# Kernel tuning notes

Hardware: AMD Instinct MI355X
Metric: run time of the kernel (lower is better)

Reference implementation:

```python
import jax, jax.numpy as jnp
import numpy as np

B, S, D = 1, 2048, 2048
H, KV, HD = 32, 8, 64          # heads, kv heads, head_dim
WINDOW = 1024                  # sliding window (left), causal
ROPE_THETA = 10000.0


def setup_inputs() -> dict:
    key = jax.random.key(0)
    ks = jax.random.split(key, 5)
    scale = 1.0 / np.sqrt(D)
    x = jax.random.normal(ks[0], (B, S, D), dtype=jnp.float32)
    wq = jax.random.normal(ks[1], (D, H * HD), dtype=jnp.float32) * scale
    wk = jax.random.normal(ks[2], (D, KV * HD), dtype=jnp.float32) * scale
    wv = jax.random.normal(ks[3], (D, KV * HD), dtype=jnp.float32) * scale
    wo = jax.random.normal(ks[4], (H * HD, D), dtype=jnp.float32) * scale
    # RoPE frequencies: freqs_cis = exp(i * t * theta^{-2j/hd}), stored as cos/sin
    inv_freq = 1.0 / (ROPE_THETA ** (np.arange(0, HD, 2, dtype=np.float32) / HD))  # [HD/2]
    t = np.arange(S, dtype=np.float32)
    ang = np.outer(t, inv_freq)  # [S, HD/2]
    freqs_cos = jnp.asarray(np.cos(ang), dtype=jnp.float32)
    freqs_sin = jnp.asarray(np.sin(ang), dtype=jnp.float32)
    return {"x": x, "wq": wq, "wk": wk, "wv": wv, "wo": wo,
            "freqs_cos": freqs_cos, "freqs_sin": freqs_sin}


def _apply_rope(t, cos, sin):
    # t: [B,S,h,HD]; pairs (t[...,2i], t[...,2i+1]) form complex numbers
    tr = t.reshape(*t.shape[:-1], HD // 2, 2)
    a, b = tr[..., 0], tr[..., 1]
    c = cos[None, :, None, :]  # [1,S,1,HD/2]
    s = sin[None, :, None, :]
    ra = a * c - b * s
    rb = a * s + b * c
    return jnp.stack([ra, rb], axis=-1).reshape(t.shape)


def reference(x, wq, wk, wv, wo, freqs_cos, freqs_sin):
    q = (x @ wq).reshape(B, S, H, HD)
    k = (x @ wk).reshape(B, S, KV, HD)
    v = (x @ wv).reshape(B, S, KV, HD)
    q = _apply_rope(q, freqs_cos, freqs_sin)
    k = _apply_rope(k, freqs_cos, freqs_sin)
    # GQA: repeat kv heads to match query heads
    k = jnp.repeat(k, H // KV, axis=2)  # [B,S,H,HD]
    v = jnp.repeat(v, H // KV, axis=2)
    scale = jnp.asarray(1.0 / np.sqrt(HD), dtype=x.dtype)
    scores = jnp.einsum('bqhd,bkhd->bhqk', q, k) * scale  # [B,H,S,S]
    i = jnp.arange(S)[:, None]
    j = jnp.arange(S)[None, :]
    allowed = (j <= i) & (j >= i - WINDOW)  # causal + sliding window
    scores = jnp.where(allowed[None, None], scores, jnp.asarray(-1e30, dtype=scores.dtype))
    attn = jax.nn.softmax(scores, axis=-1)
    out = jnp.einsum('bhqk,bkhd->bqhd', attn, v).reshape(B, S, H * HD)
    return out @ wo
```

## Files before the change

### kernel.cpp

```cpp
#include <hip/hip_runtime.h>
#include <stdint.h>

typedef __bf16 bf16_t;
typedef __bf16 bf16x8 __attribute__((ext_vector_type(8)));
typedef __bf16 bf16x4 __attribute__((ext_vector_type(4)));
typedef float floatx4 __attribute__((ext_vector_type(4)));

#define AS3(p) ((__attribute__((address_space(3))) void*)(p))
#define AS1(p) ((__attribute__((address_space(1))) void*)(void*)(p))

__global__ __launch_bounds__(256) void cvt_k(const float* __restrict__ src,
                                             bf16_t* __restrict__ dst, int n) {
  const int i = (blockIdx.x * 256 + threadIdx.x) * 8;
  if (i + 8 <= n) {
    floatx4 a = *(const floatx4*)&src[i];
    floatx4 b = *(const floatx4*)&src[i + 4];
    bf16x8 o;
#pragma unroll
    for (int j = 0; j < 4; ++j) { o[j] = (bf16_t)a[j]; o[4 + j] = (bf16_t)b[j]; }
    *(bf16x8*)&dst[i] = o;
  }
}

__global__ __launch_bounds__(256) void tr_k(const float* __restrict__ src, int ncols,
                                            bf16_t* __restrict__ dst) {
  __shared__ __align__(16) bf16_t T[64][68];
  const int t = threadIdx.x;
  const int nt = blockIdx.x * 64, kt = blockIdx.y * 64;
  const int r0 = t >> 4;
  const int c0 = (t & 15) << 2;
#pragma unroll
  for (int p = 0; p < 4; ++p) {
    const int row = p * 16 + r0;
    floatx4 v = *(const floatx4*)&src[(size_t)(kt + row) * ncols + nt + c0];
    bf16x4 b;
#pragma unroll
    for (int i = 0; i < 4; ++i) b[i] = (bf16_t)v[i];
    *(bf16x4*)&T[row][c0] = b;
  }
  __syncthreads();
#pragma unroll
  for (int p = 0; p < 4; ++p) {
    const int n = p * 16 + r0;
    bf16x4 tmp;
#pragma unroll
    for (int i = 0; i < 4; ++i) tmp[i] = T[c0 + i][n];
    *(bf16x4*)&dst[(size_t)(nt + n) * 2048 + kt + c0] = tmp;
  }
}

template <int EPI>
__global__ __launch_bounds__(256) void gemm_k(const bf16_t* __restrict__ A,
                                              const bf16_t* __restrict__ Bt,
                                              bf16_t* __restrict__ o0,
                                              bf16_t* __restrict__ o1,
                                              bf16_t* __restrict__ o2,
                                              float* __restrict__ fo,
                                              const float* __restrict__ fcos,
                                              const float* __restrict__ fsin) {
  constexpr int K = 2048;
  __shared__ __align__(16) bf16_t As[64 * 64];
  __shared__ __align__(16) bf16_t Bs[128 * 64];
  const int tid = threadIdx.x;
  const int lane = tid & 63;
  const int w = tid >> 6;
  const int quad = lane >> 4;
  const int l15 = lane & 15;
  const int m0 = blockIdx.y * 64;
  const int n0 = blockIdx.x * 128;
  const int sr = lane >> 3;
  const int sc = ((lane & 7) ^ (sr & 7)) << 3;
  const bf16_t* gA = A + (size_t)(m0 + w * 16 + sr) * K + sc;
  const bf16_t* gB = Bt + (size_t)(n0 + w * 32 + sr) * K + sc;
  bf16_t* lA = &As[w * 1024];
  bf16_t* lB = &Bs[w * 2048];
  floatx4 acc[4][2] = {};

  for (int k0 = 0; k0 < K; k0 += 64) {
    __builtin_amdgcn_global_load_lds(AS1(gA + k0), AS3(lA), 16, 0, 0);
    __builtin_amdgcn_global_load_lds(AS1(gA + 8 * K + k0), AS3(lA + 512), 16, 0, 0);
#pragma unroll
    for (int qq = 0; qq < 4; ++qq)
      __builtin_amdgcn_global_load_lds(AS1(gB + (size_t)qq * 8 * K + k0),
                                       AS3(lB + qq * 512), 16, 0, 0);
    __syncthreads();
#pragma unroll
    for (int kk = 0; kk < 2; ++kk) {
      const int co = ((kk * 4 + quad) ^ (l15 & 7)) << 3;
      bf16x8 af[4], bfr[2];
#pragma unroll
      for (int i = 0; i < 4; ++i) af[i] = *(const bf16x8*)&As[(i * 16 + l15) * 64 + co];
#pragma unroll
      for (int i = 0; i < 2; ++i)
        bfr[i] = *(const bf16x8*)&Bs[(w * 32 + i * 16 + l15) * 64 + co];
#pragma unroll
      for (int mi = 0; mi < 4; ++mi)
#pragma unroll
        for (int ni = 0; ni < 2; ++ni)
          acc[mi][ni] =
              __builtin_amdgcn_mfma_f32_16x16x32_bf16(af[mi], bfr[ni], acc[mi][ni], 0, 0, 0);
    }
    __syncthreads();
  }

  if constexpr (EPI == 0) {
#pragma unroll
    for (int ni = 0; ni < 2; ++ni) {
      const int col = n0 + w * 32 + ni * 16 + l15;
#pragma unroll
      for (int mi = 0; mi < 4; ++mi) {
        const int sb = m0 + mi * 16 + quad * 4;
        if (col < 2560) {
          const int fi = (col & 63) >> 1;
#pragma unroll
          for (int r = 0; r < 4; ++r) {
            const float v = acc[mi][ni][r];
            const float prt = __shfl_xor(v, 1);
            const int s = sb + r;
            const float c = fcos[s * 32 + fi];
            const float sn = fsin[s * 32 + fi];
            const float ov = (col & 1) ? (prt * sn + v * c) : (v * c - prt * sn);
            if (col < 2048)
              o0[(size_t)s * 2048 + col] = (bf16_t)ov;
            else
              o1[(size_t)s * 512 + (col - 2048)] = (bf16_t)ov;
          }
        } else {
          const int sp = (sb & ~31) | (quad * 8 + (mi & 1) * 4);
          bf16x4 pv;
#pragma unroll
          for (int r = 0; r < 4; ++r) pv[r] = (bf16_t)acc[mi][ni][r];
          *(bf16x4*)&o2[(size_t)(col - 2560) * 2048 + sp] = pv;
        }
      }
    }
  } else {
#pragma unroll
    for (int ni = 0; ni < 2; ++ni) {
      const int col = n0 + w * 32 + ni * 16 + l15;
#pragma unroll
      for (int mi = 0; mi < 4; ++mi) {
        const int sb = m0 + mi * 16 + quad * 4;
#pragma unroll
        for (int r = 0; r < 4; ++r) fo[(size_t)(sb + r) * 2048 + col] = acc[mi][ni][r];
      }
    }
  }
}

__global__ __launch_bounds__(256) void attn_k(const bf16_t* __restrict__ qb_,
                                              const bf16_t* __restrict__ kb_,
                                              const bf16_t* __restrict__ vt_,
                                              bf16_t* __restrict__ ob_) {
  __shared__ __align__(16) bf16_t sm[2][8 * 512];
  const int lane = threadIdx.x & 63, w = threadIdx.x >> 6;
  const int quad = lane >> 4, l15 = lane & 15;
  const int h = blockIdx.y, g = h >> 2;
  const int qb = (gridDim.x - 1 - blockIdx.x) * 64;
  const int qw = qb + w * 16;
  const int q = qw + l15;
  const bf16_t* qrow = qb_ + (size_t)q * 2048 + h * 64;
  const bf16x8 qf0 = *(const bf16x8*)(qrow + quad * 8);
  const bf16x8 qf1 = *(const bf16x8*)(qrow + 32 + quad * 8);
  floatx4 acc0 = {}, acc1 = {}, acc2 = {}, acc3 = {}, accl = {};
  const float SC = 0.125f * 1.44269504088896340736f;
  bf16x8 ones;
#pragma unroll
  for (int i = 0; i < 8; ++i) ones[i] = (bf16_t)1.0f;

  int kbB = qb - 1024;
  if (kbB < 0) kbB = 0;
  kbB &= ~31;
  const int nT = (qb + 64 - kbB) >> 5;
  int myS = qw - 1024;
  if (myS < 0) myS = 0;
  myS &= ~31;
  const int myE = qw + 16;

  const int lr = lane & 15, lc = lane >> 4;
  const bf16_t* gk = kb_ + (size_t)(kbB + (w >> 1) * 16 + lr) * 512 + g * 64 +
                     ((w & 1) * 4 + lc) * 8;
  const bf16_t* gv = vt_ + (size_t)(g * 64 + w * 16 + lr) * 2048 + kbB + lc * 8;

#define STAGE(bi, ti)                                                              \
  do {                                                                             \
    __builtin_amdgcn_global_load_lds(AS1(gk + (size_t)(ti) * (32 * 512)),          \
                                     AS3(&sm[bi][w * 512]), 16, 0, 0);             \
    __builtin_amdgcn_global_load_lds(AS1(gv + (size_t)(ti) * 32),                  \
                                     AS3(&sm[bi][(4 + w) * 512]), 16, 0, 0);       \
  } while (0)

#define MSK(pv, key)                                        \
  do {                                                      \
    if ((key) > q || (key) + 1024 < q) pv = -1.0e30f;       \
  } while (0)

  int kb = kbB;
  STAGE(0, 0);
  __syncthreads();
  for (int i = 0; i < nT; ++i, kb += 32) {
    if (i + 1 < nT) STAGE((i + 1) & 1, i + 1);
    if (kb >= myS && kb < myE) {
      const bf16_t* base = &sm[i & 1][(size_t)lane * 8];
      const bf16x8 k0 = *(const bf16x8*)(base);
      const bf16x8 k1 = *(const bf16x8*)(base + 512);
      const bf16x8 k2 = *(const bf16x8*)(base + 1024);
      const bf16x8 k3 = *(const bf16x8*)(base + 1536);
      const bf16x8 v0 = *(const bf16x8*)(base + 2048);
      const bf16x8 v1 = *(const bf16x8*)(base + 2560);
      const bf16x8 v2 = *(const bf16x8*)(base + 3072);
      const bf16x8 v3 = *(const bf16x8*)(base + 3584);
      floatx4 z0 = {}, z1 = {};
      z0 = __builtin_amdgcn_mfma_f32_16x16x32_bf16(k0, qf0, z0, 0, 0, 0);
      z0 = __builtin_amdgcn_mfma_f32_16x16x32_bf16(k1, qf1, z0, 0, 0, 0);
      z1 = __builtin_amdgcn_mfma_f32_16x16x32_bf16(k2, qf0, z1, 0, 0, 0);
      z1 = __builtin_amdgcn_mfma_f32_16x16x32_bf16(k3, qf1, z1, 0, 0, 0);
      float p0 = z0[0] * SC - 32.0f, p1 = z0[1] * SC - 32.0f;
      float p2 = z0[2] * SC - 32.0f, p3 = z0[3] * SC - 32.0f;
      float p4 = z1[0] * SC - 32.0f, p5 = z1[1] * SC - 32.0f;
      float p6 = z1[2] * SC - 32.0f, p7 = z1[3] * SC - 32.0f;
      if ((kb + 31 > qw) || (kb < qw - 1009)) {
        const int kq = kb + quad * 4;
        MSK(p0, kq + 0); MSK(p1, kq + 1); MSK(p2, kq + 2); MSK(p3, kq + 3);
        MSK(p4, kq + 16); MSK(p5, kq + 17); MSK(p6, kq + 18); MSK(p7, kq + 19);
      }
      bf16x8 pf;
      pf[0] = (bf16_t)__builtin_amdgcn_exp2f(p0);
      pf[1] = (bf16_t)__builtin_amdgcn_exp2f(p1);
      pf[2] = (bf16_t)__builtin_amdgcn_exp2f(p2);
      pf[3] = (bf16_t)__builtin_amdgcn_exp2f(p3);
      pf[4] = (bf16_t)__builtin_amdgcn_exp2f(p4);
      pf[5] = (bf16_t)__builtin_amdgcn_exp2f(p5);
      pf[6] = (bf16_t)__builtin_amdgcn_exp2f(p6);
      pf[7] = (bf16_t)__builtin_amdgcn_exp2f(p7);
      accl = __builtin_amdgcn_mfma_f32_16x16x32_bf16(ones, pf, accl, 0, 0, 0);
      acc0 = __builtin_amdgcn_mfma_f32_16x16x32_bf16(v0, pf, acc0, 0, 0, 0);
      acc1 = __builtin_amdgcn_mfma_f32_16x16x32_bf16(v1, pf, acc1, 0, 0, 0);
      acc2 = __builtin_amdgcn_mfma_f32_16x16x32_bf16(v2, pf, acc2, 0, 0, 0);
      acc3 = __builtin_amdgcn_mfma_f32_16x16x32_bf16(v3, pf, acc3, 0, 0, 0);
    }
    __syncthreads();
  }
#undef STAGE
#undef MSK

  const float inv = 1.0f / accl[0];
  bf16_t* obase = ob_ + (size_t)q * 2048 + h * 64 + quad * 4;
  bf16x4 ov;
#pragma unroll
  for (int r = 0; r < 4; ++r) ov[r] = (bf16_t)(acc0[r] * inv);
  *(bf16x4*)(obase) = ov;
#pragma unroll
  for (int r = 0; r < 4; ++r) ov[r] = (bf16_t)(acc1[r] * inv);
  *(bf16x4*)(obase + 16) = ov;
#pragma unroll
  for (int r = 0; r < 4; ++r) ov[r] = (bf16_t)(acc2[r] * inv);
  *(bf16x4*)(obase + 32) = ov;
#pragma unroll
  for (int r = 0; r < 4; ++r) ov[r] = (bf16_t)(acc3[r] * inv);
  *(bf16x4*)(obase + 48) = ov;
}

extern "C" void kernel_launch(void* const* d_in, const int* in_sizes, int n_in, void* d_out,
                              int out_size, void* d_ws, size_t ws_size, hipStream_t stream) {
  (void)in_sizes;
  (void)n_in;
  (void)out_size;
  (void)ws_size;
  const float* x = (const float*)d_in[0];
  const float* wq = (const float*)d_in[1];
  const float* wk = (const float*)d_in[2];
  const float* wv = (const float*)d_in[3];
  const float* wo = (const float*)d_in[4];
  const float* fcos = (const float*)d_in[5];
  const float* fsin = (const float*)d_in[6];
  float* out = (float*)d_out;

  bf16_t* xb = (bf16_t*)d_ws;
  bf16_t* wt = xb + (size_t)2048 * 2048;
  bf16_t* qbuf = wt + (size_t)5120 * 2048;
  bf16_t* kbuf = qbuf + (size_t)2048 * 2048;
  bf16_t* vtb = kbuf + (size_t)2048 * 512;
  bf16_t* att = vtb + (size_t)512 * 2048;

  cvt_k<<<2048, 256, 0, stream>>>(x, xb, 2048 * 2048);
  tr_k<<<dim3(32, 32), 256, 0, stream>>>(wq, 2048, wt);
  tr_k<<<dim3(8, 32), 256, 0, stream>>>(wk, 512, wt + (size_t)2048 * 2048);
  tr_k<<<dim3(8, 32), 256, 0, stream>>>(wv, 512, wt + (size_t)2560 * 2048);
  tr_k<<<dim3(32, 32), 256, 0, stream>>>(wo, 2048, wt + (size_t)3072 * 2048);
  gemm_k<0><<<dim3(24, 32), 256, 0, stream>>>(xb, wt, qbuf, kbuf, vtb, nullptr, fcos, fsin);
  attn_k<<<dim3(32, 32), 256, 0, stream>>>(qbuf, kbuf, vtb, att);
  gemm_k<1><<<dim3(16, 32), 256, 0, stream>>>(att, wt + (size_t)3072 * 2048, nullptr, nullptr,
                                              nullptr, out, fcos, fsin);
}
```

Baseline: 214.8 us.

## Fuse prep kernels into one launch and use 2-wave GEMM blocks

Merges the x conversion and four weight-transpose launches into a single prep kernel dispatched by block index, which removes launch overhead and tail gaps between the small kernels. It also changes the GEMM block from four waves, each computing a 64x32 subtile, to two waves each computing 64x64, doubling per-wave MFMA work and register accumulators. Per-thread global-to-LDS loads rise accordingly. The halved thread count per block lowers latency hiding on the same grid, and the larger accumulator set raises register pressure.

New measurement: 233.2 us. 1.09x slower.

```diff
diff --git a/kernel.cpp b/kernel.cpp
--- a/kernel.cpp
+++ b/kernel.cpp
@@ -9,24 +9,10 @@
 #define AS3(p) ((__attribute__((address_space(3))) void*)(p))
 #define AS1(p) ((__attribute__((address_space(1))) void*)(void*)(p))
 
-__global__ __launch_bounds__(256) void cvt_k(const float* __restrict__ src,
-                                             bf16_t* __restrict__ dst, int n) {
-  const int i = (blockIdx.x * 256 + threadIdx.x) * 8;
-  if (i + 8 <= n) {
-    floatx4 a = *(const floatx4*)&src[i];
-    floatx4 b = *(const floatx4*)&src[i + 4];
-    bf16x8 o;
-#pragma unroll
-    for (int j = 0; j < 4; ++j) { o[j] = (bf16_t)a[j]; o[4 + j] = (bf16_t)b[j]; }
-    *(bf16x8*)&dst[i] = o;
-  }
-}
-
-__global__ __launch_bounds__(256) void tr_k(const float* __restrict__ src, int ncols,
-                                            bf16_t* __restrict__ dst) {
-  __shared__ __align__(16) bf16_t T[64][68];
-  const int t = threadIdx.x;
-  const int nt = blockIdx.x * 64, kt = blockIdx.y * 64;
+__device__ __forceinline__ void tr_dev(const float* __restrict__ src, int ncols,
+                                       bf16_t* __restrict__ dst, int bx, int by, int t,
+                                       bf16_t (*T)[68]) {
+  const int nt = bx * 64, kt = by * 64;
   const int r0 = t >> 4;
   const int c0 = (t & 15) << 2;
 #pragma unroll
@@ -49,8 +35,40 @@
   }
 }
 
+__global__ __launch_bounds__(256) void prep_k(const float* __restrict__ x,
+                                              const float* __restrict__ wq,
+                                              const float* __restrict__ wk,
+                                              const float* __restrict__ wv,
+                                              const float* __restrict__ wo,
+                                              bf16_t* __restrict__ xb,
+                                              bf16_t* __restrict__ wt) {
+  __shared__ __align__(16) bf16_t T[64][68];
+  const int b = blockIdx.x, tid = threadIdx.x;
+  if (b < 2048) {
+    const int i = (b * 256 + tid) * 8;
+    floatx4 a = *(const floatx4*)&x[i];
+    floatx4 c = *(const floatx4*)&x[i + 4];
+    bf16x8 o;
+#pragma unroll
+    for (int j = 0; j < 4; ++j) { o[j] = (bf16_t)a[j]; o[4 + j] = (bf16_t)c[j]; }
+    *(bf16x8*)&xb[i] = o;
+  } else if (b < 3072) {
+    const int t = b - 2048;
+    tr_dev(wq, 2048, wt, t & 31, t >> 5, tid, T);
+  } else if (b < 3328) {
+    const int t = b - 3072;
+    tr_dev(wk, 512, wt + (size_t)2048 * 2048, t & 7, t >> 3, tid, T);
+  } else if (b < 3584) {
+    const int t = b - 3328;
+    tr_dev(wv, 512, wt + (size_t)2560 * 2048, t & 7, t >> 3, tid, T);
+  } else {
+    const int t = b - 3584;
+    tr_dev(wo, 2048, wt + (size_t)3072 * 2048, t & 31, t >> 5, tid, T);
+  }
+}
+
 template <int EPI>
-__global__ __launch_bounds__(256) void gemm_k(const bf16_t* __restrict__ A,
+__global__ __launch_bounds__(128) void gemm_k(const bf16_t* __restrict__ A,
                                               const bf16_t* __restrict__ Bt,
                                               bf16_t* __restrict__ o0,
                                               bf16_t* __restrict__ o1,
@@ -70,33 +88,35 @@
   const int n0 = blockIdx.x * 128;
   const int sr = lane >> 3;
   const int sc = ((lane & 7) ^ (sr & 7)) << 3;
-  const bf16_t* gA = A + (size_t)(m0 + w * 16 + sr) * K + sc;
-  const bf16_t* gB = Bt + (size_t)(n0 + w * 32 + sr) * K + sc;
-  bf16_t* lA = &As[w * 1024];
-  bf16_t* lB = &Bs[w * 2048];
-  floatx4 acc[4][2] = {};
+  const bf16_t* gA = A + (size_t)(m0 + w * 32 + sr) * K + sc;
+  const bf16_t* gB = Bt + (size_t)(n0 + w * 64 + sr) * K + sc;
+  bf16_t* lA = &As[(w * 32) * 64];
+  bf16_t* lB = &Bs[(w * 64) * 64];
+  floatx4 acc[4][4] = {};
 
   for (int k0 = 0; k0 < K; k0 += 64) {
-    __builtin_amdgcn_global_load_lds(AS1(gA + k0), AS3(lA), 16, 0, 0);
-    __builtin_amdgcn_global_load_lds(AS1(gA + 8 * K + k0), AS3(lA + 512), 16, 0, 0);
-#pragma unroll
-    for (int qq = 0; qq < 4; ++qq)
-      __builtin_amdgcn_global_load_lds(AS1(gB + (size_t)qq * 8 * K + k0),
-                                       AS3(lB + qq * 512), 16, 0, 0);
+#pragma unroll
+    for (int j = 0; j < 4; ++j)
+      __builtin_amdgcn_global_load_lds(AS1(gA + (size_t)j * 8 * K + k0),
+                                       AS3(lA + j * 8 * 64), 16, 0, 0);
+#pragma unroll
+    for (int j = 0; j < 8; ++j)
+      __builtin_amdgcn_global_load_lds(AS1(gB + (size_t)j * 8 * K + k0),
+                                       AS3(lB + j * 8 * 64), 16, 0, 0);
     __syncthreads();
 #pragma unroll
     for (int kk = 0; kk < 2; ++kk) {
       const int co = ((kk * 4 + quad) ^ (l15 & 7)) << 3;
-      bf16x8 af[4], bfr[2];
-#pragma unroll
-      for (int i = 0; i < 4; ++i) af[i] = *(const bf16x8*)&As[(i * 16 + l15) * 64 + co];
-#pragma unroll
-      for (int i = 0; i < 2; ++i)
-        bfr[i] = *(const bf16x8*)&Bs[(w * 32 + i * 16 + l15) * 64 + co];
+      bf16x8 af[4], bfr[4];
+#pragma unroll
+      for (int i = 0; i < 4; ++i) {
+        af[i] = *(const bf16x8*)&As[(i * 16 + l15) * 64 + co];
+        bfr[i] = *(const bf16x8*)&Bs[(w * 64 + i * 16 + l15) * 64 + co];
+      }
 #pragma unroll
       for (int mi = 0; mi < 4; ++mi)
 #pragma unroll
-        for (int ni = 0; ni < 2; ++ni)
+        for (int ni = 0; ni < 4; ++ni)
           acc[mi][ni] =
               __builtin_amdgcn_mfma_f32_16x16x32_bf16(af[mi], bfr[ni], acc[mi][ni], 0, 0, 0);
     }
@@ -105,8 +125,8 @@
 
   if constexpr (EPI == 0) {
 #pragma unroll
-    for (int ni = 0; ni < 2; ++ni) {
-      const int col = n0 + w * 32 + ni * 16 + l15;
+    for (int ni = 0; ni < 4; ++ni) {
+      const int col = n0 + w * 64 + ni * 16 + l15;
 #pragma unroll
       for (int mi = 0; mi < 4; ++mi) {
         const int sb = m0 + mi * 16 + quad * 4;
@@ -136,8 +156,8 @@
     }
   } else {
 #pragma unroll
-    for (int ni = 0; ni < 2; ++ni) {
-      const int col = n0 + w * 32 + ni * 16 + l15;
+    for (int ni = 0; ni < 4; ++ni) {
+      const int col = n0 + w * 64 + ni * 16 + l15;
 #pragma unroll
       for (int mi = 0; mi < 4; ++mi) {
         const int sb = m0 + mi * 16 + quad * 4;
@@ -283,13 +303,9 @@
   bf16_t* vtb = kbuf + (size_t)2048 * 512;
   bf16_t* att = vtb + (size_t)512 * 2048;
 
-  cvt_k<<<2048, 256, 0, stream>>>(x, xb, 2048 * 2048);
-  tr_k<<<dim3(32, 32), 256, 0, stream>>>(wq, 2048, wt);
-  tr_k<<<dim3(8, 32), 256, 0, stream>>>(wk, 512, wt + (size_t)2048 * 2048);
-  tr_k<<<dim3(8, 32), 256, 0, stream>>>(wv, 512, wt + (size_t)2560 * 2048);
-  tr_k<<<dim3(32, 32), 256, 0, stream>>>(wo, 2048, wt + (size_t)3072 * 2048);
-  gemm_k<0><<<dim3(24, 32), 256, 0, stream>>>(xb, wt, qbuf, kbuf, vtb, nullptr, fcos, fsin);
+  prep_k<<<4608, 256, 0, stream>>>(x, wq, wk, wv, wo, xb, wt);
+  gemm_k<0><<<dim3(24, 32), 128, 0, stream>>>(xb, wt, qbuf, kbuf, vtb, nullptr, fcos, fsin);
   attn_k<<<dim3(32, 32), 256, 0, stream>>>(qbuf, kbuf, vtb, att);
-  gemm_k<1><<<dim3(16, 32), 256, 0, stream>>>(att, wt + (size_t)3072 * 2048, nullptr, nullptr,
+  gemm_k<1><<<dim3(16, 32), 128, 0, stream>>>(att, wt + (size_t)3072 * 2048, nullptr, nullptr,
                                               nullptr, out, fcos, fsin);
 }
```
